# Performance work log

Measured on AMD Instinct MI355X. Metric: run time of the kernel, lower is better.

The kernel has to match this reference:

```python
import jax, jax.numpy as jnp
import numpy as np

V, E, H, D = 32000, 512, 512, 512  # vocab, emb_dim, enc_hid_dim, dec_hid_dim
B, S, T = 32, 64, 48               # batch, src_len, trg_len


def _gru_cell(x, h, Wih, Whh, bih, bhh):
    # PyTorch GRU cell semantics (gate order r, z, n)
    gi = x @ Wih.T + bih
    gh = h @ Whh.T + bhh
    ir, iz, i_n = jnp.split(gi, 3, axis=-1)
    hr, hz, h_n = jnp.split(gh, 3, axis=-1)
    r = jax.nn.sigmoid(ir + hr)
    z = jax.nn.sigmoid(iz + hz)
    n = jnp.tanh(i_n + r * h_n)
    return (1.0 - z) * n + z * h


def setup_inputs() -> dict:
    key = jax.random.key(0)
    ks = jax.random.split(key, 21)
    f = lambda k, shp: jax.random.normal(k, shp, dtype=jnp.float32) * 0.05
    inp = {
        'src': jax.random.randint(ks[0], (B, S), 0, V),
        'trg': jax.random.randint(ks[1], (T, B), 0, V),
        'emb': f(ks[2], (V, E)),
        'encf_Wih': f(ks[3], (3 * H, E)), 'encf_Whh': f(ks[4], (3 * H, H)),
        'encf_bih': f(ks[5], (3 * H,)), 'encf_bhh': f(ks[6], (3 * H,)),
        'encb_Wih': f(ks[7], (3 * H, E)), 'encb_Whh': f(ks[8], (3 * H, H)),
        'encb_bih': f(ks[9], (3 * H,)), 'encb_bhh': f(ks[10], (3 * H,)),
        'fc_W': f(ks[11], (D, 2 * H)), 'fc_b': f(ks[12], (D,)),
        'attn_W': f(ks[13], (D, D + 2 * H)), 'attn_v': f(ks[14], (D,)),
        'dec_Wih': f(ks[15], (3 * D, E + 2 * H)), 'dec_Whh': f(ks[16], (3 * D, D)),
        'dec_bih': f(ks[17], (3 * D,)), 'dec_bhh': f(ks[18], (3 * D,)),
        'out_W': f(ks[19], (V, 2 * H + D + E)),
        'out_b': jnp.zeros((V,), dtype=jnp.float32),
    }
    return inp


def _forward(src, trg, emb, encf_Wih, encf_Whh, encf_bih, encf_bhh,
             encb_Wih, encb_Whh, encb_bih, encb_bhh, fc_W, fc_b,
             attn_W, attn_v, dec_Wih, dec_Whh, dec_bih, dec_bhh, out_W, out_b):
    x = emb[src]                       # [B,S,E]
    xT = jnp.swapaxes(x, 0, 1)         # [S,B,E]
    h0 = jnp.zeros((src.shape[0], encf_Whh.shape[1]), dtype=x.dtype)

    def stepf(h, xt):
        h2 = _gru_cell(xt, h, encf_Wih, encf_Whh, encf_bih, encf_bhh)
        return h2, h2

    def stepb(h, xt):
        h2 = _gru_cell(xt, h, encb_Wih, encb_Whh, encb_bih, encb_bhh)
        return h2, h2

    hf, yf = jax.lax.scan(stepf, h0, xT)
    hb, yb = jax.lax.scan(stepb, h0, xT[::-1])
    # [B,S,2H] bidirectional encoder outputs (backward stream re-reversed)
    enc_out = jnp.concatenate([jnp.swapaxes(yf, 0, 1), jnp.swapaxes(yb[::-1], 0, 1)], axis=-1)
    # decoder init state from final fwd/bwd hidden
    s0 = jnp.tanh(jnp.concatenate([hf, hb], axis=-1) @ fc_W.T + fc_b)  # [B,D]

    def dec_step(s, tok):
        e = emb[tok]  # [B,E]
        srep = jnp.broadcast_to(s[:, None, :], (s.shape[0], enc_out.shape[1], s.shape[1]))
        energy = jnp.tanh(jnp.concatenate([srep, enc_out], axis=-1) @ attn_W.T)  # [B,S,D]
        a = jax.nn.softmax(energy @ attn_v, axis=1)  # [B,S]
        c = jnp.einsum('bs,bsh->bh', a, enc_out)     # [B,2H]
        s2 = _gru_cell(jnp.concatenate([e, c], axis=-1), s, dec_Wih, dec_Whh, dec_bih, dec_bhh)
        pred = jnp.concatenate([s2, c, e], axis=-1) @ out_W.T + out_b  # [B,V]
        return s2, pred

    # teacher forcing: decoder inputs are trg[0..T-2]
    _, preds = jax.lax.scan(dec_step, s0, trg[:-1])
    out0 = jnp.zeros((1,) + preds.shape[1:], dtype=preds.dtype)  # outputs[0] stays zero
    return jnp.concatenate([out0, preds], axis=0)  # [T,B,V]


def reference(src, trg, emb, encf_Wih, encf_Whh, encf_bih, encf_bhh,
              encb_Wih, encb_Whh, encb_bih, encb_bhh, fc_W, fc_b,
              attn_W, attn_v, dec_Wih, dec_Whh, dec_bih, dec_bhh, out_W, out_b):
    return _forward(src, trg, emb, encf_Wih, encf_Whh, encf_bih, encf_bhh,
                    encb_Wih, encb_Whh, encb_bih, encb_bhh, fc_W, fc_b,
                    attn_W, attn_v, dec_Wih, dec_Whh, dec_bih, dec_bhh, out_W, out_b)
```

## Files before the change

kernel.cpp:

```cpp
#include <hip/hip_runtime.h>
#include <stdint.h>
#include <stddef.h>

typedef __attribute__((ext_vector_type(8))) short short8;
typedef __attribute__((ext_vector_type(4))) float f32x4;
typedef unsigned int u32;

__device__ inline unsigned short f2bf(float f) {
  union { float f; uint32_t u; } v; v.f = f;
  uint32_t u = v.u;
  u += 0x7FFFu + ((u >> 16) & 1u);
  return (unsigned short)(u >> 16);
}
__device__ inline float bf2f(unsigned short h) {
  union { uint32_t u; float f; } v; v.u = ((uint32_t)h) << 16; return v.f;
}
__device__ inline short8 pack8(float4 a, float4 b) {
  short8 r;
  r[0] = (short)f2bf(a.x); r[1] = (short)f2bf(a.y);
  r[2] = (short)f2bf(a.z); r[3] = (short)f2bf(a.w);
  r[4] = (short)f2bf(b.x); r[5] = (short)f2bf(b.y);
  r[6] = (short)f2bf(b.z); r[7] = (short)f2bf(b.w);
  return r;
}
__device__ inline float tanh_fast(float x) {
  float xc = fminf(fmaxf(x, -9.f), 9.f);
  float e = __expf(2.f * xc);
  return (e - 1.f) * __builtin_amdgcn_rcpf(e + 1.f);
}
__device__ inline float sigm_fast(float x) {
  float xc = fminf(fmaxf(x, -30.f), 30.f);
  return __builtin_amdgcn_rcpf(1.f + __expf(-xc));
}
__device__ inline void gl_lds16(const unsigned short* g, unsigned short* l) {
  __builtin_amdgcn_global_load_lds(
      (const __attribute__((address_space(1))) u32*)g,
      (__attribute__((address_space(3))) u32*)l, 16, 0, 0);
}

__global__ __launch_bounds__(128) void prep_gather(
    const int* __restrict__ src, const int* __restrict__ trg,
    const float* __restrict__ emb,
    unsigned short* __restrict__ xbf, unsigned short* __restrict__ ebf,
    unsigned short* __restrict__ Zbf) {
  int r = blockIdx.x, tid = threadIdx.x;
  if (r < 2048) {
    int b = r & 31, s = r >> 5;
    int tok = src[b * 64 + s];
    const float* e = emb + (size_t)tok * 512;
    float4 v = *(const float4*)(e + tid * 4);
    unsigned short* dst = xbf + (size_t)r * 512 + tid * 4;
    dst[0] = f2bf(v.x); dst[1] = f2bf(v.y); dst[2] = f2bf(v.z); dst[3] = f2bf(v.w);
  } else {
    int rr = r - 2048;
    int t = rr >> 5, b = rr & 31;
    unsigned short* dst = ebf + (size_t)rr * 512 + tid * 4;
    if (t < 47) {
      int tok = trg[t * 32 + b];
      const float* e = emb + (size_t)tok * 512;
      float4 v = *(const float4*)(e + tid * 4);
      unsigned short q0 = f2bf(v.x), q1 = f2bf(v.y), q2 = f2bf(v.z), q3 = f2bf(v.w);
      dst[0] = q0; dst[1] = q1; dst[2] = q2; dst[3] = q3;
      unsigned short* zd = Zbf + (size_t)rr * 2048 + 1536 + tid * 4;
      zd[0] = q0; zd[1] = q1; zd[2] = q2; zd[3] = q3;
    } else {
      dst[0] = 0; dst[1] = 0; dst[2] = 0; dst[3] = 0;
    }
  }
}

__global__ __launch_bounds__(256) void cvt_f32_bf16(const float* __restrict__ src,
                                                    unsigned short* __restrict__ dst,
                                                    long long n4) {
  long long i = (long long)blockIdx.x * 256 + threadIdx.x;
  long long stride = (long long)gridDim.x * 256;
  for (; i < n4; i += stride) {
    float4 v = ((const float4*)src)[i];
    unsigned short* d = dst + i * 4;
    d[0] = f2bf(v.x); d[1] = f2bf(v.y); d[2] = f2bf(v.z); d[3] = f2bf(v.w);
  }
}

__global__ __launch_bounds__(64) void cvt_rows(const float* __restrict__ src, int srcld,
                                               unsigned short* __restrict__ dst) {
  int r = blockIdx.x, c = threadIdx.x * 8;
  const float* s = src + (size_t)r * srcld + c;
  *(short8*)(dst + (size_t)r * 512 + c) = pack8(*(const float4*)s, *(const float4*)(s + 4));
}

template <bool ABF, bool BBF, bool WBF>
__global__ __launch_bounds__(256) void gemm_kernel(
    const void* __restrict__ Av, int lda,
    const void* __restrict__ Bv, int ldb, int bco,
    const float* __restrict__ bias,
    void* __restrict__ Cv, int ldc,
    int K, int Mvalid, int row_off) {
  __shared__ __align__(16) unsigned short As[128 * 32];
  __shared__ __align__(16) unsigned short Bs[128 * 32];
  const int tid = threadIdx.x;
  const int m0 = blockIdx.x * 128, n0 = blockIdx.y * 128;
  const int w = tid >> 6, lane = tid & 63;
  const int wm = w >> 1, wn = w & 1;
  const int fr = lane & 15, fq = lane >> 4;
  f32x4 acc[4][4];
#pragma unroll
  for (int mi = 0; mi < 4; ++mi)
#pragma unroll
    for (int ni = 0; ni < 4; ++ni) acc[mi][ni] = (f32x4){0.f, 0.f, 0.f, 0.f};
  for (int k0 = 0; k0 < K; k0 += 32) {
#pragma unroll
    for (int p = 0; p < 2; ++p) {
      int idx = p * 256 + tid;
      int row = idx >> 2, seg = idx & 3;
      if (ABF) {
        const unsigned short* Ab = (const unsigned short*)Av;
        *(short8*)(As + row * 32 + seg * 8) =
            *(const short8*)(Ab + (size_t)(m0 + row) * lda + k0 + seg * 8);
      } else {
        const float* Af = (const float*)Av;
        const float* ap = Af + (size_t)(m0 + row) * lda + k0 + seg * 8;
        *(short8*)(As + row * 32 + seg * 8) = pack8(*(const float4*)ap, *(const float4*)(ap + 4));
      }
      if (BBF) {
        const unsigned short* Bb = (const unsigned short*)Bv;
        *(short8*)(Bs + row * 32 + seg * 8) =
            *(const short8*)(Bb + (size_t)(n0 + row) * ldb + bco + k0 + seg * 8);
      } else {
        const float* Bf = (const float*)Bv;
        const float* bp = Bf + (size_t)(n0 + row) * ldb + bco + k0 + seg * 8;
        *(short8*)(Bs + row * 32 + seg * 8) = pack8(*(const float4*)bp, *(const float4*)(bp + 4));
      }
    }
    __syncthreads();
    short8 af[4], bfr[4];
#pragma unroll
    for (int mi = 0; mi < 4; ++mi)
      af[mi] = *(const short8*)(As + (wm * 64 + mi * 16 + fr) * 32 + fq * 8);
#pragma unroll
    for (int ni = 0; ni < 4; ++ni)
      bfr[ni] = *(const short8*)(Bs + (wn * 64 + ni * 16 + fr) * 32 + fq * 8);
#pragma unroll
    for (int mi = 0; mi < 4; ++mi)
#pragma unroll
      for (int ni = 0; ni < 4; ++ni)
        acc[mi][ni] = __builtin_amdgcn_mfma_f32_16x16x32_bf16(af[mi], bfr[ni], acc[mi][ni], 0, 0, 0);
    __syncthreads();
  }
#pragma unroll
  for (int mi = 0; mi < 4; ++mi)
#pragma unroll
    for (int ni = 0; ni < 4; ++ni) {
      int col = n0 + wn * 64 + ni * 16 + fr;
      float bv = bias ? bias[col] : 0.f;
#pragma unroll
      for (int j = 0; j < 4; ++j) {
        int rowm = m0 + wm * 64 + mi * 16 + fq * 4 + j;
        if (rowm < Mvalid) {
          float val = acc[mi][ni][j] + bv;
          if (WBF)
            ((unsigned short*)Cv)[(size_t)(rowm + row_off) * ldc + col] = f2bf(val);
          else
            ((float*)Cv)[(size_t)(rowm + row_off) * ldc + col] = val;
        }
      }
    }
}

__global__ __launch_bounds__(256) void gemm_big(
    const unsigned short* __restrict__ A, int lda,
    const unsigned short* __restrict__ B, int ldb,
    const float* __restrict__ bias,
    float* __restrict__ C, int ldc,
    int K, int Mvalid, int row_off) {
  __shared__ __align__(16) unsigned short As[128 * 32];
  __shared__ __align__(16) unsigned short Bs[128 * 32];
  const int tid = threadIdx.x;
  int wg = blockIdx.x;
  wg = (wg & 7) * 375 + (wg >> 3);
  const int m0 = (wg % 12) * 128, n0 = (wg / 12) * 128;
  const int w = tid >> 6, lane = tid & 63;
  const int wm = w >> 1, wn = w & 1;
  const int fr = lane & 15, fq = lane >> 4;
  const int srow = lane >> 2, sseg = lane & 3;
  f32x4 acc[4][4];
#pragma unroll
  for (int mi = 0; mi < 4; ++mi)
#pragma unroll
    for (int ni = 0; ni < 4; ++ni) acc[mi][ni] = (f32x4){0.f, 0.f, 0.f, 0.f};
  for (int k0 = 0; k0 < K; k0 += 32) {
#pragma unroll
    for (int c = 0; c < 2; ++c) {
      int row = w * 32 + c * 16 + srow;
      gl_lds16(A + (size_t)(m0 + row) * lda + k0 + sseg * 8, As + row * 32);
      gl_lds16(B + (size_t)(n0 + row) * ldb + k0 + sseg * 8, Bs + row * 32);
    }
    __syncthreads();
    short8 af[4], bfr[4];
#pragma unroll
    for (int mi = 0; mi < 4; ++mi)
      af[mi] = *(const short8*)(As + (wm * 64 + mi * 16 + fr) * 32 + fq * 8);
#pragma unroll
    for (int ni = 0; ni < 4; ++ni)
      bfr[ni] = *(const short8*)(Bs + (wn * 64 + ni * 16 + fr) * 32 + fq * 8);
#pragma unroll
    for (int mi = 0; mi < 4; ++mi)
#pragma unroll
      for (int ni = 0; ni < 4; ++ni)
        acc[mi][ni] = __builtin_amdgcn_mfma_f32_16x16x32_bf16(af[mi], bfr[ni], acc[mi][ni], 0, 0, 0);
    __syncthreads();
  }
#pragma unroll
  for (int mi = 0; mi < 4; ++mi)
#pragma unroll
    for (int ni = 0; ni < 4; ++ni) {
      int col = n0 + wn * 64 + ni * 16 + fr;
      float bv = bias[col];
#pragma unroll
      for (int j = 0; j < 4; ++j) {
        int rowm = m0 + wm * 64 + mi * 16 + fq * 4 + j;
        if (rowm < Mvalid) C[(size_t)(rowm + row_off) * ldc + col] = acc[mi][ni][j] + bv;
      }
    }
}

__global__ __launch_bounds__(512) void enc_step(
    const float* __restrict__ Gif, const float* __restrict__ Gib,
    const unsigned short* __restrict__ whFbf, const unsigned short* __restrict__ whBbf,
    const float* __restrict__ bhhF, const float* __restrict__ bhhB,
    unsigned short* __restrict__ hbf,
    float* __restrict__ hf32,
    unsigned short* __restrict__ ebo,
    float* __restrict__ hcat,
    const float* __restrict__ outW, unsigned short* __restrict__ outWbf, int nCvt,
    int t) {
  const int blk = blockIdx.x, tid = threadIdx.x;
  if (blk >= 32) {
    if (blk - 32 < nCvt) {
      size_t base4 = ((size_t)t * nCvt + (blk - 32)) * 1280;
      for (int i = tid; i < 1280; i += 512) {
        float4 v = ((const float4*)outW)[base4 + i];
        unsigned short* d = outWbf + (base4 + i) * 4;
        d[0] = f2bf(v.x); d[1] = f2bf(v.y); d[2] = f2bf(v.z); d[3] = f2bf(v.w);
      }
    }
    return;
  }
  const int dir = blk >> 4, slice = blk & 15, D0 = slice * 32;
  const unsigned short* Wbf = dir ? whBbf : whFbf;
  const float* Gi = dir ? Gib : Gif;
  const float* bhh = dir ? bhhB : bhhF;
  __shared__ __align__(16) unsigned short hlds[32 * 520];
  __shared__ __align__(16) float gl[96 * 33];
  const unsigned short* hb = hbf + dir * 32768 + (t & 1) * 16384;
  for (int c = tid; c < 32 * 64; c += 512) {
    int r = c >> 6, seg = c & 63;
    *(short8*)(hlds + r * 520 + seg * 8) = *(const short8*)(hb + r * 512 + seg * 8);
  }
  __syncthreads();
  const int w = tid >> 6, lane = tid & 63, fr = lane & 15, fq = lane >> 4;
  if (w < 6) {
    int row = w * 16 + fr;
    int gr = (row >> 5) * 512 + D0 + (row & 31);
    const unsigned short* wrow = Wbf + (size_t)gr * 512;
    f32x4 acc0 = {0.f, 0.f, 0.f, 0.f}, acc1 = {0.f, 0.f, 0.f, 0.f};
#pragma unroll
    for (int k0 = 0; k0 < 512; k0 += 32) {
      short8 bq = *(const short8*)(wrow + k0 + fq * 8);
      short8 a0 = *(const short8*)(hlds + fr * 520 + k0 + fq * 8);
      short8 a1 = *(const short8*)(hlds + (16 + fr) * 520 + k0 + fq * 8);
      acc0 = __builtin_amdgcn_mfma_f32_16x16x32_bf16(a0, bq, acc0, 0, 0, 0);
      acc1 = __builtin_amdgcn_mfma_f32_16x16x32_bf16(a1, bq, acc1, 0, 0, 0);
    }
#pragma unroll
    for (int j = 0; j < 4; ++j) {
      gl[row * 33 + fq * 4 + j] = acc0[j];
      gl[row * 33 + 16 + fq * 4 + j] = acc1[j];
    }
  }
  __syncthreads();
  const int srow = dir ? 63 - t : t;
  unsigned short* hnb = hbf + dir * 32768 + ((t + 1) & 1) * 16384;
  const float* hcur = hf32 + dir * 32768 + (t & 1) * 16384;
  float* hnf = hf32 + dir * 32768 + ((t + 1) & 1) * 16384;
#pragma unroll
  for (int rep = 0; rep < 2; ++rep) {
    int idx = rep * 512 + tid, b = idx >> 5, dl = idx & 31, d = D0 + dl;
    float ar = gl[dl * 33 + b] + bhh[d];
    float az = gl[(32 + dl) * 33 + b] + bhh[512 + d];
    float an = gl[(64 + dl) * 33 + b] + bhh[1024 + d];
    const float* gi = Gi + ((size_t)srow * 32 + b) * 1536;
    float r = sigm_fast(gi[d] + ar);
    float z = sigm_fast(gi[512 + d] + az);
    float n = tanh_fast(gi[1024 + d] + r * an);
    float h2 = (1.f - z) * n + z * hcur[b * 512 + d];
    hnb[b * 512 + d] = f2bf(h2);
    hnf[b * 512 + d] = h2;
    ebo[((size_t)b * 64 + srow) * 1024 + (size_t)dir * 512 + d] = f2bf(h2);
    if (t == 63) hcat[(size_t)b * 1024 + (size_t)dir * 512 + d] = h2;
  }
}

__global__ __launch_bounds__(512) void tanh_s0(const float* __restrict__ s0raw,
                                               float* __restrict__ sf32,
                                               unsigned short* __restrict__ sbf) {
  int idx = blockIdx.x * 512 + threadIdx.x;
  float v = tanhf(s0raw[idx]);
  sf32[idx] = v;
  sbf[idx] = f2bf(v);
}

__global__ __launch_bounds__(512) void dec_proj(
    const unsigned short* __restrict__ Wcat, const float* __restrict__ decBhh,
    const unsigned short* __restrict__ sbf, float* __restrict__ gout, int t) {
  const int g = blockIdx.x, tid = threadIdx.x;
  __shared__ __align__(16) unsigned short slds[32 * 520];
  const unsigned short* sb = sbf + (t & 1) * 16384;
  for (int c = tid; c < 32 * 64; c += 512) {
    int r = c >> 6, seg = c & 63;
    *(short8*)(slds + r * 520 + seg * 8) = *(const short8*)(sb + r * 512 + seg * 8);
  }
  __syncthreads();
  const int w = tid >> 6, lane = tid & 63, fr = lane & 15, fq = lane >> 4;
  const int mt = w >> 2, nt = w & 3;
  int rc = g * 64 + nt * 16 + fr;
  const unsigned short* wrow = Wcat + (size_t)rc * 512;
  f32x4 acc = {0.f, 0.f, 0.f, 0.f};
#pragma unroll
  for (int k0 = 0; k0 < 512; k0 += 32) {
    short8 a = *(const short8*)(slds + (mt * 16 + fr) * 520 + k0 + fq * 8);
    short8 bq = *(const short8*)(wrow + k0 + fq * 8);
    acc = __builtin_amdgcn_mfma_f32_16x16x32_bf16(a, bq, acc, 0, 0, 0);
  }
  float bv = rc < 512 ? 0.f : decBhh[rc - 512];
#pragma unroll
  for (int j = 0; j < 4; ++j)
    gout[(size_t)(mt * 16 + fq * 4 + j) * 2048 + rc] = acc[j] + bv;
}

__global__ __launch_bounds__(512) void dec_attn(
    const float* __restrict__ attnV,
    const unsigned short* __restrict__ epf, const unsigned short* __restrict__ ebo,
    const unsigned short* __restrict__ EP2b, const float* __restrict__ Gie,
    const float* __restrict__ gout,
    unsigned short* __restrict__ sbf, float* __restrict__ sf32,
    unsigned short* __restrict__ Zbf, int t) {
  const int b = blockIdx.x, tid = threadIdx.x;
  __shared__ __align__(16) float gout_f[2048];
  __shared__ float raw[64], aaw[64];
  __shared__ float vlds[512];
  vlds[tid] = attnV[tid];
  *(float4*)(gout_f + tid * 4) = *(const float4*)(gout + (size_t)b * 2048 + tid * 4);
  __syncthreads();
  const int s_i = tid >> 3, l8 = tid & 7;
  {
    float part = 0.f;
    const float* gp = gout_f + l8 * 64;
    const unsigned short* ep = epf + ((size_t)b * 64 + s_i) * 512 + l8 * 64;
    const float* vv = vlds + l8 * 64;
#pragma unroll
    for (int jc = 0; jc < 8; ++jc) {
      short8 e8 = *(const short8*)(ep + jc * 8);
      float4 g0 = *(const float4*)(gp + jc * 8);
      float4 g1 = *(const float4*)(gp + jc * 8 + 4);
      float4 v0 = *(const float4*)(vv + jc * 8);
      float4 v1 = *(const float4*)(vv + jc * 8 + 4);
      part += tanh_fast(g0.x + bf2f((unsigned short)e8[0])) * v0.x;
      part += tanh_fast(g0.y + bf2f((unsigned short)e8[1])) * v0.y;
      part += tanh_fast(g0.z + bf2f((unsigned short)e8[2])) * v0.z;
      part += tanh_fast(g0.w + bf2f((unsigned short)e8[3])) * v0.w;
      part += tanh_fast(g1.x + bf2f((unsigned short)e8[4])) * v1.x;
      part += tanh_fast(g1.y + bf2f((unsigned short)e8[5])) * v1.y;
      part += tanh_fast(g1.z + bf2f((unsigned short)e8[6])) * v1.z;
      part += tanh_fast(g1.w + bf2f((unsigned short)e8[7])) * v1.w;
    }
    part += __shfl_xor(part, 1);
    part += __shfl_xor(part, 2);
    part += __shfl_xor(part, 4);
    if (l8 == 0) raw[s_i] = part;
  }
  __syncthreads();
  if (tid < 64) {
    float x = raw[tid];
    float m = x;
#pragma unroll
    for (int k = 1; k < 64; k <<= 1) m = fmaxf(m, __shfl_xor(m, k));
    float e = __expf(x - m);
    float s = e;
#pragma unroll
    for (int k = 1; k < 64; k <<= 1) s += __shfl_xor(s, k);
    aaw[tid] = e * __builtin_amdgcn_rcpf(s);
  }
  __syncthreads();
  float c0 = 0.f, c1 = 0.f, g0a = 0.f, g1a = 0.f, g2a = 0.f;
  {
    const unsigned short* eb = ebo + (size_t)b * 64 * 1024 + tid;
    const unsigned short* e2 = EP2b + (size_t)b * 64 * 1536 + tid;
#pragma unroll 8
    for (int s2 = 0; s2 < 64; ++s2) {
      float a = aaw[s2];
      c0 += a * bf2f(eb[(size_t)s2 * 1024]);
      c1 += a * bf2f(eb[(size_t)s2 * 1024 + 512]);
      g0a += a * bf2f(e2[(size_t)s2 * 1536]);
      g1a += a * bf2f(e2[(size_t)s2 * 1536 + 512]);
      g2a += a * bf2f(e2[(size_t)s2 * 1536 + 1024]);
    }
  }
  const float* gie = Gie + ((size_t)t * 32 + b) * 1536;
  float sprev = sf32[(t & 1) * 16384 + b * 512 + tid];
  float rr = sigm_fast(gie[tid] + g0a + gout_f[512 + tid]);
  float zz = sigm_fast(gie[512 + tid] + g1a + gout_f[1024 + tid]);
  float nn = tanh_fast(gie[1024 + tid] + g2a + rr * gout_f[1536 + tid]);
  float s2v = (1.f - zz) * nn + zz * sprev;
  sbf[((t + 1) & 1) * 16384 + b * 512 + tid] = f2bf(s2v);
  sf32[((t + 1) & 1) * 16384 + b * 512 + tid] = s2v;
  size_t zrow = ((size_t)t * 32 + b) * 2048;
  Zbf[zrow + tid] = f2bf(s2v);
  Zbf[zrow + 512 + tid] = f2bf(c0);
  Zbf[zrow + 1024 + tid] = f2bf(c1);
}

extern "C" void kernel_launch(void* const* d_in, const int* in_sizes, int n_in,
                              void* d_out, int out_size, void* d_ws, size_t ws_size,
                              hipStream_t stream) {
  (void)in_sizes; (void)n_in; (void)out_size;
  const int* src = (const int*)d_in[0];
  const int* trg = (const int*)d_in[1];
  const float* emb = (const float*)d_in[2];
  const float* encf_Wih = (const float*)d_in[3];
  const float* encf_Whh = (const float*)d_in[4];
  const float* encf_bih = (const float*)d_in[5];
  const float* encf_bhh = (const float*)d_in[6];
  const float* encb_Wih = (const float*)d_in[7];
  const float* encb_Whh = (const float*)d_in[8];
  const float* encb_bih = (const float*)d_in[9];
  const float* encb_bhh = (const float*)d_in[10];
  const float* fc_W = (const float*)d_in[11];
  const float* fc_b = (const float*)d_in[12];
  const float* attn_W = (const float*)d_in[13];
  const float* attn_v = (const float*)d_in[14];
  const float* dec_Wih = (const float*)d_in[15];
  const float* dec_Whh = (const float*)d_in[16];
  const float* dec_bih = (const float*)d_in[17];
  const float* dec_bhh = (const float*)d_in[18];
  const float* out_W = (const float*)d_in[19];
  const float* out_b = (const float*)d_in[20];
  float* out = (float*)d_out;

  char* p = (char*)d_ws;
  size_t off = 0;
  auto alloc = [&](size_t bytes) {
    void* r = p + off;
    off = (off + bytes + 255) & ~(size_t)255;
    return r;
  };
  unsigned short* xbf = (unsigned short*)alloc((size_t)2048 * 512 * 2);
  unsigned short* ebf = (unsigned short*)alloc((size_t)1536 * 512 * 2);
  unsigned short* Zbf = (unsigned short*)alloc((size_t)1536 * 2048 * 2);
  float* Gif = (float*)alloc((size_t)2048 * 1536 * 4);
  float* Gib = (float*)alloc((size_t)2048 * 1536 * 4);
  float* Gie = (float*)alloc((size_t)1536 * 1536 * 4);
  unsigned short* ebo = (unsigned short*)alloc((size_t)2048 * 1024 * 2);
  unsigned short* epf = (unsigned short*)alloc((size_t)2048 * 512 * 2);
  unsigned short* EP2b = (unsigned short*)alloc((size_t)2048 * 1536 * 2);
  unsigned short* whFbf = (unsigned short*)alloc((size_t)1536 * 512 * 2);
  unsigned short* whBbf = (unsigned short*)alloc((size_t)1536 * 512 * 2);
  unsigned short* Wcat = (unsigned short*)alloc((size_t)2048 * 512 * 2);
  unsigned short* hbf = (unsigned short*)alloc((size_t)2 * 2 * 32 * 512 * 2);
  float* hf32 = (float*)alloc((size_t)2 * 2 * 32 * 512 * 4);
  float* hcat = (float*)alloc((size_t)32 * 1024 * 4);
  float* s0raw = (float*)alloc((size_t)32 * 512 * 4);
  unsigned short* sbf = (unsigned short*)alloc((size_t)2 * 32 * 512 * 2);
  float* sf32 = (float*)alloc((size_t)2 * 32 * 512 * 4);
  float* gout = (float*)alloc((size_t)32 * 2048 * 4);
  unsigned short* outWbf = (unsigned short*)alloc((size_t)32000 * 2048 * 2);
  const bool bigB = (off <= ws_size);

  hipMemsetAsync(hbf, 0, (size_t)2 * 2 * 32 * 512 * 2, stream);
  hipMemsetAsync(hf32, 0, (size_t)2 * 2 * 32 * 512 * 4, stream);
  hipMemsetAsync(d_out, 0, (size_t)32 * 32000 * 4, stream);

  prep_gather<<<3584, 128, 0, stream>>>(src, trg, emb, xbf, ebf, Zbf);
  cvt_rows<<<1536, 64, 0, stream>>>(encf_Whh, 512, whFbf);
  cvt_rows<<<1536, 64, 0, stream>>>(encb_Whh, 512, whBbf);
  cvt_rows<<<512, 64, 0, stream>>>(attn_W, 1536, Wcat);
  cvt_rows<<<1536, 64, 0, stream>>>(dec_Whh, 512, Wcat + (size_t)512 * 512);

  gemm_kernel<true, false, false><<<dim3(16, 12), 256, 0, stream>>>(
      xbf, 512, encf_Wih, 512, 0, encf_bih, Gif, 1536, 512, 2048, 0);
  gemm_kernel<true, false, false><<<dim3(16, 12), 256, 0, stream>>>(
      xbf, 512, encb_Wih, 512, 0, encb_bih, Gib, 1536, 512, 2048, 0);
  gemm_kernel<true, false, false><<<dim3(12, 12), 256, 0, stream>>>(
      ebf, 512, dec_Wih, 1536, 0, dec_bih, Gie, 1536, 512, 1536, 0);

  const int nCvt = bigB ? 200 : 0;
  for (int t = 0; t < 64; ++t)
    enc_step<<<32 + nCvt, 512, 0, stream>>>(Gif, Gib, whFbf, whBbf, encf_bhh, encb_bhh,
                                            hbf, hf32, ebo, hcat, out_W, outWbf, nCvt, t);

  gemm_kernel<false, false, false><<<dim3(1, 4), 256, 0, stream>>>(
      hcat, 1024, fc_W, 1024, 0, fc_b, s0raw, 512, 1024, 32, 0);
  tanh_s0<<<32, 512, 0, stream>>>(s0raw, sf32, sbf);

  gemm_kernel<true, false, true><<<dim3(16, 4), 256, 0, stream>>>(
      ebo, 1024, attn_W, 1536, 512, nullptr, epf, 512, 1024, 2048, 0);
  gemm_kernel<true, false, true><<<dim3(16, 12), 256, 0, stream>>>(
      ebo, 1024, dec_Wih, 1536, 512, nullptr, EP2b, 1536, 1024, 2048, 0);

  for (int t = 0; t < 47; ++t) {
    dec_proj<<<32, 512, 0, stream>>>(Wcat, dec_bhh, sbf, gout, t);
    dec_attn<<<32, 512, 0, stream>>>(attn_v, epf, ebo, EP2b, Gie, gout,
                                     sbf, sf32, Zbf, t);
  }

  if (bigB)
    gemm_big<<<3000, 256, 0, stream>>>(Zbf, 2048, outWbf, 2048, out_b,
                                       out, 32000, 2048, 1504, 32);
  else
    gemm_kernel<true, false, false><<<dim3(12, 250), 256, 0, stream>>>(
        Zbf, 2048, out_W, 2048, 0, out_b, out, 32000, 2048, 1504, 32);
}
```

Measured before the change: 1.982 ms.

## Replace output-projection GEMM with 256x256-tile double-buffered swizzled LDS kernel

Swaps the 128x128-tile, single-buffered output projection GEMM (3000 blocks of 256 threads) for a 256x256-tile kernel with 512 threads. It uses 128KB of dynamic LDS with double buffering over K-tiles of 64 and an XOR swizzle to avoid bank conflicts. Loads for the next K-tile are interleaved with MFMA work, and s_setprio is used around the MFMA bursts. The aim is more data reuse per block and hiding global-load latency in this vocab-sized projection. The cost is one block per CU, hard-coded shapes, and a tail where 750 blocks do not divide evenly across CUs. The unused cvt_f32_bf16 kernel is also removed.

```diff
diff --git a/kernel.cpp b/kernel.cpp
--- a/kernel.cpp
+++ b/kernel.cpp
@@ -69,18 +69,6 @@
   }
 }
 
-__global__ __launch_bounds__(256) void cvt_f32_bf16(const float* __restrict__ src,
-                                                    unsigned short* __restrict__ dst,
-                                                    long long n4) {
-  long long i = (long long)blockIdx.x * 256 + threadIdx.x;
-  long long stride = (long long)gridDim.x * 256;
-  for (; i < n4; i += stride) {
-    float4 v = ((const float4*)src)[i];
-    unsigned short* d = dst + i * 4;
-    d[0] = f2bf(v.x); d[1] = f2bf(v.y); d[2] = f2bf(v.z); d[3] = f2bf(v.w);
-  }
-}
-
 __global__ __launch_bounds__(64) void cvt_rows(const float* __restrict__ src, int srcld,
                                                unsigned short* __restrict__ dst) {
   int r = blockIdx.x, c = threadIdx.x * 8;
@@ -166,59 +154,111 @@
     }
 }
 
-__global__ __launch_bounds__(256) void gemm_big(
-    const unsigned short* __restrict__ A, int lda,
-    const unsigned short* __restrict__ B, int ldb,
+__global__ __launch_bounds__(512, 1) void gemm_big8(
+    const unsigned short* __restrict__ A,
+    const unsigned short* __restrict__ B,
     const float* __restrict__ bias,
-    float* __restrict__ C, int ldc,
-    int K, int Mvalid, int row_off) {
-  __shared__ __align__(16) unsigned short As[128 * 32];
-  __shared__ __align__(16) unsigned short Bs[128 * 32];
+    float* __restrict__ C) {
+  extern __shared__ char lds[];
+  char* LA = lds;
+  char* LB = lds + 65536;
   const int tid = threadIdx.x;
+  const int w = tid >> 6, lane = tid & 63;
   int wg = blockIdx.x;
-  wg = (wg & 7) * 375 + (wg >> 3);
-  const int m0 = (wg % 12) * 128, n0 = (wg / 12) * 128;
-  const int w = tid >> 6, lane = tid & 63;
-  const int wm = w >> 1, wn = w & 1;
+  {
+    int x = wg & 7, i = wg >> 3;
+    wg = (x < 6 ? x * 94 : 564 + (x - 6) * 93) + i;
+  }
+  const int m0 = (wg % 6) * 256, n0 = (wg / 6) * 256;
+  const int wm = w >> 2, wn = w & 3;
   const int fr = lane & 15, fq = lane >> 4;
-  const int srow = lane >> 2, sseg = lane & 3;
-  f32x4 acc[4][4];
-#pragma unroll
-  for (int mi = 0; mi < 4; ++mi)
+
+  auto stage = [&](const unsigned short* G, char* L, int rowbase, int kt, int h, int c) {
+#pragma unroll
+    for (int j = 0; j < 2; ++j) {
+      int pbh = j * 8192 + w * 1024;
+      int pl = pbh + lane * 16;
+      int lb = pl ^ (((pl >> 9) & 1) << 5);
+      int rl = lb >> 7, ch = (lb >> 4) & 7;
+      gl_lds16(G + (size_t)(rowbase + h * 128 + rl) * 2048 + kt * 64 + ch * 8,
+               (unsigned short*)(L + c * 32768 + h * 16384 + pbh));
+    }
+  };
+
+  f32x4 acc[8][4];
+#pragma unroll
+  for (int mi = 0; mi < 8; ++mi)
 #pragma unroll
     for (int ni = 0; ni < 4; ++ni) acc[mi][ni] = (f32x4){0.f, 0.f, 0.f, 0.f};
-  for (int k0 = 0; k0 < K; k0 += 32) {
-#pragma unroll
-    for (int c = 0; c < 2; ++c) {
-      int row = w * 32 + c * 16 + srow;
-      gl_lds16(A + (size_t)(m0 + row) * lda + k0 + sseg * 8, As + row * 32);
-      gl_lds16(B + (size_t)(n0 + row) * ldb + k0 + sseg * 8, Bs + row * 32);
-    }
-    __syncthreads();
-    short8 af[4], bfr[4];
-#pragma unroll
-    for (int mi = 0; mi < 4; ++mi)
-      af[mi] = *(const short8*)(As + (wm * 64 + mi * 16 + fr) * 32 + fq * 8);
-#pragma unroll
-    for (int ni = 0; ni < 4; ++ni)
-      bfr[ni] = *(const short8*)(Bs + (wn * 64 + ni * 16 + fr) * 32 + fq * 8);
-#pragma unroll
-    for (int mi = 0; mi < 4; ++mi)
-#pragma unroll
-      for (int ni = 0; ni < 4; ++ni)
-        acc[mi][ni] = __builtin_amdgcn_mfma_f32_16x16x32_bf16(af[mi], bfr[ni], acc[mi][ni], 0, 0, 0);
-    __syncthreads();
-  }
-#pragma unroll
-  for (int mi = 0; mi < 4; ++mi)
+
+  stage(A, LA, m0, 0, 0, 0); stage(B, LB, n0, 0, 0, 0);
+  stage(A, LA, m0, 0, 1, 0); stage(B, LB, n0, 0, 1, 0);
+  asm volatile("s_waitcnt vmcnt(0)" ::: "memory");
+  __builtin_amdgcn_s_barrier();
+
+  short8 bfrag[8];
+  for (int kt = 0; kt < 32; ++kt) {
+    const int c = kt & 1;
+    char* Abuf = LA + c * 32768;
+    char* Bbuf = LB + c * 32768;
+#pragma unroll
+    for (int p = 0; p < 4; ++p) {
+      if (kt < 31) {
+        if (p == 0) {
+          stage(A, LA, m0, kt + 1, 0, c ^ 1);
+          stage(B, LB, n0, kt + 1, 0, c ^ 1);
+        } else if (p == 1) {
+          stage(A, LA, m0, kt + 1, 1, c ^ 1);
+          stage(B, LB, n0, kt + 1, 1, c ^ 1);
+        }
+      }
+      if (p == 0) {
+#pragma unroll
+        for (int ni = 0; ni < 4; ++ni)
+#pragma unroll
+          for (int ks = 0; ks < 2; ++ks) {
+            int n = wn * 64 + ni * 16 + fr;
+            int h = n >> 7, nl = n & 127;
+            int lb = nl * 128 + ks * 64 + fq * 16;
+            int pb = lb ^ (((lb >> 9) & 1) << 5);
+            bfrag[ni * 2 + ks] = *(const short8*)(Bbuf + h * 16384 + pb);
+          }
+      }
+      short8 afrag[4];
+#pragma unroll
+      for (int q = 0; q < 2; ++q)
+#pragma unroll
+        for (int ks = 0; ks < 2; ++ks) {
+          int r = wm * 128 + (2 * p + q) * 16 + fr;
+          int h = r >> 7, rl = r & 127;
+          int lb = rl * 128 + ks * 64 + fq * 16;
+          int pb = lb ^ (((lb >> 9) & 1) << 5);
+          afrag[q * 2 + ks] = *(const short8*)(Abuf + h * 16384 + pb);
+        }
+      __builtin_amdgcn_s_setprio(1);
+#pragma unroll
+      for (int q = 0; q < 2; ++q)
+#pragma unroll
+        for (int ni = 0; ni < 4; ++ni)
+#pragma unroll
+          for (int ks = 0; ks < 2; ++ks)
+            acc[2 * p + q][ni] = __builtin_amdgcn_mfma_f32_16x16x32_bf16(
+                afrag[q * 2 + ks], bfrag[ni * 2 + ks], acc[2 * p + q][ni], 0, 0, 0);
+      __builtin_amdgcn_s_setprio(0);
+      if (p == 3) asm volatile("s_waitcnt vmcnt(0)" ::: "memory");
+      __builtin_amdgcn_s_barrier();
+    }
+  }
+#pragma unroll
+  for (int mi = 0; mi < 8; ++mi)
 #pragma unroll
     for (int ni = 0; ni < 4; ++ni) {
       int col = n0 + wn * 64 + ni * 16 + fr;
       float bv = bias[col];
 #pragma unroll
       for (int j = 0; j < 4; ++j) {
-        int rowm = m0 + wm * 64 + mi * 16 + fq * 4 + j;
-        if (rowm < Mvalid) C[(size_t)(rowm + row_off) * ldc + col] = acc[mi][ni][j] + bv;
+        int row = m0 + wm * 128 + mi * 16 + fq * 4 + j;
+        if (row < 1504) C[(size_t)(row + 32) * 32000 + col] = acc[mi][ni][j] + bv;
       }
     }
 }
@@ -512,10 +552,12 @@
                                      sbf, sf32, Zbf, t);
   }
 
-  if (bigB)
-    gemm_big<<<3000, 256, 0, stream>>>(Zbf, 2048, outWbf, 2048, out_b,
-                                       out, 32000, 2048, 1504, 32);
-  else
+  if (bigB) {
+    hipFuncSetAttribute((const void*)gemm_big8,
+                        hipFuncAttributeMaxDynamicSharedMemorySize, 131072);
+    gemm_big8<<<750, 512, 131072, stream>>>(Zbf, outWbf, out_b, out);
+  } else {
     gemm_kernel<true, false, false><<<dim3(12, 250), 256, 0, stream>>>(
         Zbf, 2048, out_W, 2048, 0, out_b, out, 32000, 2048, 1504, 32);
-}
+  }
+}
```

Measured after the change: 1.888 ms. -4.7%, faster.
